# Kernel optimization log

Hardware: AMD Instinct MI355X
Metric: run time of the kernel (lower is better)

The kernel has to match this reference:

```python
import jax, jax.numpy as jnp
import numpy as np

ROPE_BASE = 10000.0

def _rope_cos_sin(T, d, dtype):
    inv_freq = 1.0 / (ROPE_BASE ** (jnp.arange(0, d, 2, dtype=jnp.float32) / d))
    t = jnp.arange(T, dtype=jnp.float32)
    freqs = t[:, None] * inv_freq[None, :]           # [T, d/2]
    emb = jnp.concatenate([freqs, freqs], axis=-1)   # [T, d]
    return jnp.cos(emb).astype(dtype), jnp.sin(emb).astype(dtype)

def _rotate_half(x):
    x1, x2 = jnp.split(x, 2, axis=-1)
    return jnp.concatenate([-x2, x1], axis=-1)

def setup_inputs() -> dict:
    key = jax.random.key(0)
    k1, k2, k3, k4 = jax.random.split(key, 4)
    B, T, C, H = 4, 4096, 1024, 64
    x = jax.random.normal(k1, (B, T, C), dtype=jnp.float32)
    s = 1.0 / np.sqrt(C)
    Wq = jax.random.normal(k2, (H, C), dtype=jnp.float32) * s
    Wk = jax.random.normal(k3, (H, C), dtype=jnp.float32) * s
    Wv = jax.random.normal(k4, (H, C), dtype=jnp.float32) * s
    return {"x": x, "Wq": Wq, "Wk": Wk, "Wv": Wv}

def reference(x, Wq, Wk, Wv):
    B, T, C = x.shape
    H = Wq.shape[0]
    q = jnp.einsum('btc,hc->bth', x, Wq)
    k = jnp.einsum('btc,hc->bth', x, Wk)
    v = jnp.einsum('btc,hc->bth', x, Wv)
    cos, sin = _rope_cos_sin(T, H, x.dtype)
    q = q * cos + _rotate_half(q) * sin
    k = k * cos + _rotate_half(k) * sin
    # NOTE: original scales by dim_model**-0.5 (C), not head_size
    wei = jnp.einsum('bth,bsh->bts', q, k) * (C ** -0.5)
    causal = jnp.tril(jnp.ones((T, T), dtype=bool))
    wei = jnp.where(causal, wei, -jnp.inf)
    wei = jax.nn.softmax(wei, axis=-1)
    # dropout p=0.0 (identity)
    out = jnp.einsum('bts,bsh->bth', wei, v)
    return out
```

## Files before the change

kernel.cpp:

```cpp
#include <hip/hip_runtime.h>
#include <hip/hip_bf16.h>
#include <math.h>

typedef __attribute__((ext_vector_type(8))) __bf16 bf16x8;
typedef __attribute__((ext_vector_type(4))) float f32x4;
typedef __attribute__((ext_vector_type(16))) float f32x16;
typedef __attribute__((ext_vector_type(4))) float float4_t;
typedef __attribute__((ext_vector_type(4))) unsigned int uint4_t;

#define NB 4
#define TSEQ 4096
#define CD 1024
#define HD 64
#define NCH 16
#define CHT 4
#define QBL 16

static __device__ __forceinline__ unsigned short f2bf(float f) {
    union { float f; unsigned u; } v; v.f = f;
    unsigned r = v.u + 0x7fffu + ((v.u >> 16) & 1u);
    return (unsigned short)(r >> 16);
}
static __device__ __forceinline__ float bf2f(unsigned short u) {
    union { unsigned int i; float f; } v; v.i = ((unsigned int)u) << 16;
    return v.f;
}
static __device__ __forceinline__ unsigned int pk2(float a, float b) {
    union { __bf16 h[2]; unsigned int u; } x;
    x.h[0] = (__bf16)a; x.h[1] = (__bf16)b;
    return x.u;
}

__global__ __launch_bounds__(256) void wcvt_kernel(const float* __restrict__ wq,
                                                   const float* __restrict__ wk,
                                                   const float* __restrict__ wv,
                                                   unsigned short* __restrict__ wb) {
    int i = blockIdx.x * 256 + threadIdx.x;
    int j = i >> 10;
    int col = i & 1023;
    int jb = j >> 4, off = j & 15;
    int sub = ((jb & 1) << 5) | ((jb & 2) << 3);
    int srcrow = (jb < 8) ? (sub + off) : ((jb - 8) * 16 + off);
    const float* src = (jb < 4) ? wq : ((jb < 8) ? wk : wv);
    wb[i] = f2bf(src[srcrow * 1024 + col]);
}

__global__ __launch_bounds__(256) void qkv_kernel(const float* __restrict__ x,
                                                  const unsigned short* __restrict__ wb,
                                                  unsigned short* __restrict__ qo,
                                                  unsigned short* __restrict__ ko,
                                                  unsigned short* __restrict__ vt) {
    __shared__ unsigned short xs[64][72];
    __shared__ unsigned short ws[64][72];
    const int tid = threadIdx.x;
    const int wave = tid >> 6, lane = tid & 63;
    const int lr = lane & 15;
    const int lk = (lane >> 4) << 3;
    const int rowg = (lane >> 4) << 2;
    const int row0 = blockIdx.x * 64;
    const int cbi = blockIdx.y;
    const int cb = cbi * 64;

    f32x4 acc[4];
#pragma unroll
    for (int i = 0; i < 4; ++i) acc[i] = (f32x4){0.f, 0.f, 0.f, 0.f};

    const int sr = tid >> 2;
    const int sc = (tid & 3) << 4;

    for (int k0 = 0; k0 < CD; k0 += 64) {
        __syncthreads();
        {
            const float4_t* s4 =
                reinterpret_cast<const float4_t*>(x + (size_t)(row0 + sr) * CD + k0 + sc);
            float4_t f0 = s4[0], f1 = s4[1], f2 = s4[2], f3 = s4[3];
            uint4_t w0, w1;
            w0[0] = pk2(f0[0], f0[1]); w0[1] = pk2(f0[2], f0[3]);
            w0[2] = pk2(f1[0], f1[1]); w0[3] = pk2(f1[2], f1[3]);
            w1[0] = pk2(f2[0], f2[1]); w1[1] = pk2(f2[2], f2[3]);
            w1[2] = pk2(f3[0], f3[1]); w1[3] = pk2(f3[2], f3[3]);
            *reinterpret_cast<uint4_t*>(&xs[sr][sc]) = w0;
            *reinterpret_cast<uint4_t*>(&xs[sr][sc + 8]) = w1;
        }
        {
            const uint4_t* wsrc =
                reinterpret_cast<const uint4_t*>(wb + (size_t)(cb + sr) * CD + k0 + sc);
            *reinterpret_cast<uint4_t*>(&ws[sr][sc]) = wsrc[0];
            *reinterpret_cast<uint4_t*>(&ws[sr][sc + 8]) = wsrc[1];
        }
        __syncthreads();
#pragma unroll
        for (int kk = 0; kk < 2; ++kk) {
            bf16x8 a = *reinterpret_cast<const bf16x8*>(&xs[wave * 16 + lr][kk * 32 + lk]);
#pragma unroll
            for (int c = 0; c < 4; ++c) {
                bf16x8 bfr = *reinterpret_cast<const bf16x8*>(&ws[c * 16 + lr][kk * 32 + lk]);
                acc[c] = __builtin_amdgcn_mfma_f32_16x16x32_bf16(a, bfr, acc[c], 0, 0, 0);
            }
        }
    }

    const int gr0 = row0 + wave * 16 + rowg;
    const int bidx = gr0 >> 12;
    const int tb = gr0 & (TSEQ - 1);
    if (cbi < 2) {
        unsigned short* o = (cbi == 0) ? qo : ko;
        const float sc2 = (cbi == 0) ? 0.045084218764560315f : 1.0f;
        const float l2b = 0.4152410118609215f;
        const float invf0 = exp2f(-(float)lr * l2b);
        const float invf1 = exp2f(-(float)(lr + 16) * l2b);
#pragma unroll
        for (int r = 0; r < 4; ++r) {
            float t = (float)(tb + r);
            float s0, c0, s1, c1;
            sincosf(t * invf0, &s0, &c0);
            sincosf(t * invf1, &s1, &c1);
            size_t ro = (size_t)(gr0 + r) * HD;
            float lo, hi;
            lo = acc[0][r]; hi = acc[1][r];
            o[ro + 0 + lr]  = f2bf((lo * c0 - hi * s0) * sc2);
            o[ro + 32 + lr] = f2bf((hi * c0 + lo * s0) * sc2);
            lo = acc[2][r]; hi = acc[3][r];
            o[ro + 16 + lr] = f2bf((lo * c1 - hi * s1) * sc2);
            o[ro + 48 + lr] = f2bf((hi * c1 + lo * s1) * sc2);
        }
    } else {
#pragma unroll
        for (int r = 0; r < 4; ++r) {
            size_t vbase = (size_t)bidx * HD * TSEQ + (size_t)(tb + r);
            vt[vbase + (size_t)(0 + lr) * TSEQ]  = f2bf(acc[0][r]);
            vt[vbase + (size_t)(16 + lr) * TSEQ] = f2bf(acc[1][r]);
            vt[vbase + (size_t)(32 + lr) * TSEQ] = f2bf(acc[2][r]);
            vt[vbase + (size_t)(48 + lr) * TSEQ] = f2bf(acc[3][r]);
        }
    }
}

__global__ __launch_bounds__(512, 4) void attn_partial(const unsigned short* __restrict__ q,
                                                       const unsigned short* __restrict__ k,
                                                       const unsigned short* __restrict__ vt,
                                                       unsigned short* __restrict__ po,
                                                       float* __restrict__ pm,
                                                       float* __restrict__ pl) {
    const int chunk = blockIdx.x, qb = blockIdx.y, b = blockIdx.z;
    const int ktend_blk = 4 * qb + 3;
    const int kt0 = chunk * CHT;
    if (kt0 > ktend_blk) return;
    const int ktend = min(ktend_blk, kt0 + CHT - 1);

    __shared__ unsigned short ks[64][72];
    __shared__ unsigned short vs[64][72];
    const int tid = threadIdx.x;
    const int wave = tid >> 6, lane = tid & 63;
    const int l31 = lane & 31;
    const int h = lane >> 5;
    const int h8 = h << 3;
    const int qrow0 = qb * 256 + wave * 32;
    const int qpos = qrow0 + l31;

    const unsigned short* qb_ = q + ((size_t)(b * TSEQ + qpos)) * HD + h8;
    bf16x8 qf[4];
#pragma unroll
    for (int s = 0; s < 4; ++s)
        qf[s] = *reinterpret_cast<const bf16x8*>(qb_ + 16 * s);

    f32x16 oacc[2];
#pragma unroll
    for (int dt = 0; dt < 2; ++dt)
#pragma unroll
        for (int r = 0; r < 16; ++r) oacc[dt][r] = 0.f;
    float mreg = -1.0e30f;
    float lsum = 0.f;

    const int srow = tid >> 3;
    const int scol = (tid & 7) << 3;
    const unsigned short* kbase = k + (size_t)b * TSEQ * HD;
    const unsigned short* vbase = vt + (size_t)b * HD * TSEQ;
    uint4_t kr, vr;

    auto loadtile = [&](int kt) {
        const int s0l = kt * 64;
        kr = *reinterpret_cast<const uint4_t*>(kbase + (size_t)(s0l + srow) * HD + scol);
        vr = *reinterpret_cast<const uint4_t*>(vbase + (size_t)srow * TSEQ + s0l + scol);
    };

    loadtile(kt0);

    for (int kt = kt0; kt <= ktend; ++kt) {
        const int s0 = kt * 64;
        __syncthreads();
        *reinterpret_cast<uint4_t*>(&ks[srow][scol]) = kr;
        *reinterpret_cast<uint4_t*>(&vs[srow][scol]) = vr;
        __syncthreads();
        if (kt < ktend) loadtile(kt + 1);

        if (s0 > qrow0 + 31) continue;

        f32x16 sacc[2];
#pragma unroll
        for (int blk = 0; blk < 2; ++blk)
#pragma unroll
            for (int r = 0; r < 16; ++r) sacc[blk][r] = 0.f;
        __builtin_amdgcn_s_setprio(1);
#pragma unroll
        for (int s = 0; s < 4; ++s) {
            bf16x8 ka = *reinterpret_cast<const bf16x8*>(&ks[l31][16 * s + h8]);
            bf16x8 kb2 = *reinterpret_cast<const bf16x8*>(&ks[32 + l31][16 * s + h8]);
            sacc[0] = __builtin_amdgcn_mfma_f32_32x32x16_bf16(ka, qf[s], sacc[0], 0, 0, 0);
            sacc[1] = __builtin_amdgcn_mfma_f32_32x32x16_bf16(kb2, qf[s], sacc[1], 0, 0, 0);
        }
        __builtin_amdgcn_s_setprio(0);

        if (s0 + 63 > qrow0) {
#pragma unroll
            for (int blk = 0; blk < 2; ++blk)
#pragma unroll
                for (int r = 0; r < 16; ++r) {
                    int kvpos = s0 + 32 * blk + (r & 3) + ((r >> 2) << 3) + (h << 2);
                    if (kvpos > qpos) sacc[blk][r] = -INFINITY;
                }
        }

        float tm[8];
#pragma unroll
        for (int r = 0; r < 8; ++r)
            tm[r] = fmaxf(fmaxf(sacc[0][r], sacc[0][r + 8]),
                          fmaxf(sacc[1][r], sacc[1][r + 8]));
#pragma unroll
        for (int r = 0; r < 4; ++r) tm[r] = fmaxf(tm[r], tm[r + 4]);
        float mx = fmaxf(fmaxf(tm[0], tm[1]), fmaxf(tm[2], tm[3]));
        mx = fmaxf(mx, __shfl_xor(mx, 32, 64));

        const bool newmax = !__all(mx <= mreg + 7.0f);
        if (newmax) {
            float mnew = fmaxf(mreg, mx);
            float corr = __builtin_amdgcn_exp2f(mreg - mnew);
            mreg = mnew;
            lsum *= corr;
#pragma unroll
            for (int dt = 0; dt < 2; ++dt)
#pragma unroll
                for (int r = 0; r < 16; ++r) oacc[dt][r] *= corr;
        }

        float pvv[2][16];
#pragma unroll
        for (int blk = 0; blk < 2; ++blk)
#pragma unroll
            for (int r = 0; r < 16; ++r)
                pvv[blk][r] = __builtin_amdgcn_exp2f(sacc[blk][r] - mreg);
        float ts[8];
#pragma unroll
        for (int r = 0; r < 8; ++r)
            ts[r] = (pvv[0][r] + pvv[0][r + 8]) + (pvv[1][r] + pvv[1][r + 8]);
#pragma unroll
        for (int r = 0; r < 4; ++r) ts[r] += ts[r + 4];
        float psum = (ts[0] + ts[1]) + (ts[2] + ts[3]);
        psum += __shfl_xor(psum, 32, 64);
        lsum += psum;

        unsigned int cw[2][4][2];
#pragma unroll
        for (int blk = 0; blk < 2; ++blk)
#pragma unroll
            for (int G = 0; G < 4; ++G) {
                cw[blk][G][0] = pk2(pvv[blk][4 * G], pvv[blk][4 * G + 1]);
                cw[blk][G][1] = pk2(pvv[blk][4 * G + 2], pvv[blk][4 * G + 3]);
            }

        const bool hif = (h == 1);
        __builtin_amdgcn_s_setprio(1);
#pragma unroll
        for (int s = 0; s < 4; ++s) {
            const int blk = s >> 1, base = (s & 1) << 1;
            unsigned int a0 = cw[blk][base][0],     a1 = cw[blk][base][1];
            unsigned int b0 = cw[blk][base + 1][0], b1 = cw[blk][base + 1][1];
            unsigned int s0w = hif ? a0 : b0;
            unsigned int s1w = hif ? a1 : b1;
            unsigned int r0 = __shfl_xor(s0w, 32, 64);
            unsigned int r1 = __shfl_xor(s1w, 32, 64);
            uint4_t pw;
            pw[0] = hif ? r0 : a0;
            pw[1] = hif ? r1 : a1;
            pw[2] = hif ? b0 : r0;
            pw[3] = hif ? b1 : r1;
            bf16x8 pfrag = *reinterpret_cast<const bf16x8*>(&pw);
            bf16x8 v0 = *reinterpret_cast<const bf16x8*>(&vs[l31][16 * s + h8]);
            bf16x8 v1 = *reinterpret_cast<const bf16x8*>(&vs[32 + l31][16 * s + h8]);
            oacc[0] = __builtin_amdgcn_mfma_f32_32x32x16_bf16(v0, pfrag, oacc[0], 0, 0, 0);
            oacc[1] = __builtin_amdgcn_mfma_f32_32x32x16_bf16(v1, pfrag, oacc[1], 0, 0, 0);
        }
        __builtin_amdgcn_s_setprio(0);
    }

    const int slot = (((b << 4) + qb) << 4) + chunk;
    unsigned short* pob = po + (size_t)slot * 16384;
#pragma unroll
    for (int dt = 0; dt < 2; ++dt)
#pragma unroll
        for (int r = 0; r < 16; ++r) {
            int d = 32 * dt + (r & 3) + ((r >> 2) << 3) + (h << 2);
            pob[d * 256 + wave * 32 + l31] = f2bf(oacc[dt][r]);
        }
    if (h == 0) {
        pm[slot * 256 + wave * 32 + l31] = mreg;
        pl[slot * 256 + wave * 32 + l31] = lsum;
    }
}

__global__ __launch_bounds__(256) void attn_combine(const unsigned short* __restrict__ po,
                                                    const float* __restrict__ pm,
                                                    const float* __restrict__ pl,
                                                    float* __restrict__ out) {
    __shared__ float sm[64][17];
    const int bq = blockIdx.x;
    const int dg = blockIdx.y;
    const int qt = bq & 63;
    const int b = bq >> 6;
    const int qb = qt >> 2, quarter = qt & 3;
    const int nch = qb + 1;
    const int qi = threadIdx.x & 63;
    const int jj = threadIdx.x >> 6;
    const int slotb = (((b << 4) + qb) << 4);
    const int qoff = quarter * 64 + qi;

    float pmv[NCH];
#pragma unroll
    for (int c = 0; c < NCH; ++c)
        pmv[c] = (c < nch) ? pm[(size_t)(slotb + c) * 256 + qoff] : -1.0e30f;
    float tmv[NCH];
#pragma unroll
    for (int c = 0; c < NCH; ++c) tmv[c] = pmv[c];
#pragma unroll
    for (int s = NCH / 2; s >= 1; s >>= 1)
#pragma unroll
        for (int c = 0; c < NCH / 2; ++c)
            if (c < s) tmv[c] = fmaxf(tmv[c], tmv[c + s]);
    const float M = tmv[0];

    float L = 0.f;
    float a0 = 0.f, a1 = 0.f, a2 = 0.f, a3 = 0.f;
    const int dbase = dg * 16 + jj * 4;
#pragma unroll 4
    for (int c = 0; c < nch; ++c) {
        float w = exp2f(pmv[c] - M);
        L += w * pl[(size_t)(slotb + c) * 256 + qoff];
        const unsigned short* p = po + (size_t)(slotb + c) * 16384 + dbase * 256 + qoff;
        a0 += w * bf2f(p[0]);
        a1 += w * bf2f(p[256]);
        a2 += w * bf2f(p[512]);
        a3 += w * bf2f(p[768]);
    }
    const float inv = 1.f / L;
    sm[qi][jj * 4 + 0] = a0 * inv;
    sm[qi][jj * 4 + 1] = a1 * inv;
    sm[qi][jj * 4 + 2] = a2 * inv;
    sm[qi][jj * 4 + 3] = a3 * inv;
    __syncthreads();
    const int row = threadIdx.x >> 2;
    const int c4 = (threadIdx.x & 3) << 2;
    float4_t f;
#pragma unroll
    for (int e = 0; e < 4; ++e) f[e] = sm[row][c4 + e];
    *reinterpret_cast<float4_t*>(out + (size_t)bq * 4096 + row * 64 + dg * 16 + c4) = f;
}

extern "C" void kernel_launch(void* const* d_in, const int* in_sizes, int n_in,
                              void* d_out, int out_size, void* d_ws, size_t ws_size,
                              hipStream_t stream) {
    const float* x = (const float*)d_in[0];
    const float* wq = (const float*)d_in[1];
    const float* wk = (const float*)d_in[2];
    const float* wv = (const float*)d_in[3];
    float* out = (float*)d_out;

    unsigned short* wb = (unsigned short*)d_ws;
    unsigned short* qb = wb + 3 * HD * CD;
    unsigned short* kb = qb + (size_t)NB * TSEQ * HD;
    unsigned short* vtb = kb + (size_t)NB * TSEQ * HD;
    unsigned short* pob = vtb + (size_t)NB * TSEQ * HD;
    float* pm = (float*)(pob + (size_t)1024 * 16384);
    float* pl = pm + (size_t)1024 * 256;

    wcvt_kernel<<<768, 256, 0, stream>>>(wq, wk, wv, wb);
    qkv_kernel<<<dim3(256, 3), 256, 0, stream>>>(x, wb, qb, kb, vtb);
    attn_partial<<<dim3(NCH, QBL, NB), 512, 0, stream>>>(qb, kb, vtb, pob, pm, pl);
    attn_combine<<<dim3(NB * 64, 4), 256, 0, stream>>>(pob, pm, pl, out);
}
```

Before: 63.25 us.

## Fuse weight conversion into QKV projection and split output into two 96-column phases

Removes the separate weight-conversion kernel. Weights are now read as fp32 and converted to bf16 inside the QKV projection. The projection grid shrinks from three 64-column blocks to two 96-column blocks, so x is re-read and re-converted twice instead of three times, and the RoPE outputs for Q/K are split across the two phases. In exchange, each block does more per-iteration weight loading and conversion from fp32, uses more accumulators, and launches fewer blocks.

After: 64.17 us. About the same (+1.5%).

```diff
diff --git a/kernel.cpp b/kernel.cpp
--- a/kernel.cpp
+++ b/kernel.cpp
@@ -31,42 +31,49 @@
     return x.u;
 }
 
-__global__ __launch_bounds__(256) void wcvt_kernel(const float* __restrict__ wq,
-                                                   const float* __restrict__ wk,
-                                                   const float* __restrict__ wv,
-                                                   unsigned short* __restrict__ wb) {
-    int i = blockIdx.x * 256 + threadIdx.x;
-    int j = i >> 10;
-    int col = i & 1023;
-    int jb = j >> 4, off = j & 15;
-    int sub = ((jb & 1) << 5) | ((jb & 2) << 3);
-    int srcrow = (jb < 8) ? (sub + off) : ((jb - 8) * 16 + off);
-    const float* src = (jb < 4) ? wq : ((jb < 8) ? wk : wv);
-    wb[i] = f2bf(src[srcrow * 1024 + col]);
-}
-
 __global__ __launch_bounds__(256) void qkv_kernel(const float* __restrict__ x,
-                                                  const unsigned short* __restrict__ wb,
+                                                  const float* __restrict__ wq,
+                                                  const float* __restrict__ wk,
+                                                  const float* __restrict__ wv,
                                                   unsigned short* __restrict__ qo,
                                                   unsigned short* __restrict__ ko,
                                                   unsigned short* __restrict__ vt) {
     __shared__ unsigned short xs[64][72];
-    __shared__ unsigned short ws[64][72];
+    __shared__ unsigned short ws[96][72];
     const int tid = threadIdx.x;
     const int wave = tid >> 6, lane = tid & 63;
     const int lr = lane & 15;
     const int lk = (lane >> 4) << 3;
     const int rowg = (lane >> 4) << 2;
     const int row0 = blockIdx.x * 64;
-    const int cbi = blockIdx.y;
-    const int cb = cbi * 64;
-
-    f32x4 acc[4];
-#pragma unroll
-    for (int i = 0; i < 4; ++i) acc[i] = (f32x4){0.f, 0.f, 0.f, 0.f};
+    const int phase = blockIdx.y;
+
+    f32x4 acc[6];
+#pragma unroll
+    for (int i = 0; i < 6; ++i) acc[i] = (f32x4){0.f, 0.f, 0.f, 0.f};
 
     const int sr = tid >> 2;
     const int sc = (tid & 3) << 4;
+
+    const float* wsrcp[3];
+    int wr_[3], wc_[3];
+#pragma unroll
+    for (int i = 0; i < 3; ++i) {
+        int u = tid + (i << 8);
+        int r = u >> 3, c = (u & 7) << 3;
+        wr_[i] = r; wc_[i] = c;
+        const float* srcp; int srcrow;
+        if (phase == 0) {
+            int jb = r >> 4, off = r & 15;
+            int sub = ((jb & 1) << 5) | ((jb & 2) << 3);
+            srcp = (jb < 4) ? wq : wk;
+            srcrow = sub + off;
+        } else {
+            if (r < 32) { srcp = wk; srcrow = 16 + ((r >> 4) << 5) + (r & 15); }
+            else        { srcp = wv; srcrow = r - 32; }
+        }
+        wsrcp[i] = srcp + (size_t)srcrow * CD + c;
+    }
 
     for (int k0 = 0; k0 < CD; k0 += 64) {
         __syncthreads();
@@ -82,18 +89,21 @@
             *reinterpret_cast<uint4_t*>(&xs[sr][sc]) = w0;
             *reinterpret_cast<uint4_t*>(&xs[sr][sc + 8]) = w1;
         }
-        {
-            const uint4_t* wsrc =
-                reinterpret_cast<const uint4_t*>(wb + (size_t)(cb + sr) * CD + k0 + sc);
-            *reinterpret_cast<uint4_t*>(&ws[sr][sc]) = wsrc[0];
-            *reinterpret_cast<uint4_t*>(&ws[sr][sc + 8]) = wsrc[1];
+#pragma unroll
+        for (int i = 0; i < 3; ++i) {
+            const float4_t* s4 = reinterpret_cast<const float4_t*>(wsrcp[i] + k0);
+            float4_t f0 = s4[0], f1 = s4[1];
+            uint4_t w;
+            w[0] = pk2(f0[0], f0[1]); w[1] = pk2(f0[2], f0[3]);
+            w[2] = pk2(f1[0], f1[1]); w[3] = pk2(f1[2], f1[3]);
+            *reinterpret_cast<uint4_t*>(&ws[wr_[i]][wc_[i]]) = w;
         }
         __syncthreads();
 #pragma unroll
         for (int kk = 0; kk < 2; ++kk) {
             bf16x8 a = *reinterpret_cast<const bf16x8*>(&xs[wave * 16 + lr][kk * 32 + lk]);
 #pragma unroll
-            for (int c = 0; c < 4; ++c) {
+            for (int c = 0; c < 6; ++c) {
                 bf16x8 bfr = *reinterpret_cast<const bf16x8*>(&ws[c * 16 + lr][kk * 32 + lk]);
                 acc[c] = __builtin_amdgcn_mfma_f32_16x16x32_bf16(a, bfr, acc[c], 0, 0, 0);
             }
@@ -103,35 +113,37 @@
     const int gr0 = row0 + wave * 16 + rowg;
     const int bidx = gr0 >> 12;
     const int tb = gr0 & (TSEQ - 1);
-    if (cbi < 2) {
-        unsigned short* o = (cbi == 0) ? qo : ko;
-        const float sc2 = (cbi == 0) ? 0.045084218764560315f : 1.0f;
-        const float l2b = 0.4152410118609215f;
-        const float invf0 = exp2f(-(float)lr * l2b);
-        const float invf1 = exp2f(-(float)(lr + 16) * l2b);
-#pragma unroll
-        for (int r = 0; r < 4; ++r) {
-            float t = (float)(tb + r);
-            float s0, c0, s1, c1;
-            sincosf(t * invf0, &s0, &c0);
-            sincosf(t * invf1, &s1, &c1);
-            size_t ro = (size_t)(gr0 + r) * HD;
+    const float sc2 = 0.045084218764560315f;
+    const float l2b = 0.4152410118609215f;
+    const float invf0 = exp2f(-(float)lr * l2b);
+    const float invf1 = exp2f(-(float)(lr + 16) * l2b);
+#pragma unroll
+    for (int r = 0; r < 4; ++r) {
+        float t = (float)(tb + r);
+        float s0, c0, s1, c1;
+        sincosf(t * invf0, &s0, &c0);
+        sincosf(t * invf1, &s1, &c1);
+        size_t ro = (size_t)(gr0 + r) * HD;
+        if (phase == 0) {
             float lo, hi;
             lo = acc[0][r]; hi = acc[1][r];
-            o[ro + 0 + lr]  = f2bf((lo * c0 - hi * s0) * sc2);
-            o[ro + 32 + lr] = f2bf((hi * c0 + lo * s0) * sc2);
+            qo[ro + 0 + lr]  = f2bf((lo * c0 - hi * s0) * sc2);
+            qo[ro + 32 + lr] = f2bf((hi * c0 + lo * s0) * sc2);
             lo = acc[2][r]; hi = acc[3][r];
-            o[ro + 16 + lr] = f2bf((lo * c1 - hi * s1) * sc2);
-            o[ro + 48 + lr] = f2bf((hi * c1 + lo * s1) * sc2);
-        }
-    } else {
-#pragma unroll
-        for (int r = 0; r < 4; ++r) {
+            qo[ro + 16 + lr] = f2bf((lo * c1 - hi * s1) * sc2);
+            qo[ro + 48 + lr] = f2bf((hi * c1 + lo * s1) * sc2);
+            lo = acc[4][r]; hi = acc[5][r];
+            ko[ro + 0 + lr]  = f2bf(lo * c0 - hi * s0);
+            ko[ro + 32 + lr] = f2bf(hi * c0 + lo * s0);
+        } else {
+            float lo = acc[0][r], hi = acc[1][r];
+            ko[ro + 16 + lr] = f2bf(lo * c1 - hi * s1);
+            ko[ro + 48 + lr] = f2bf(hi * c1 + lo * s1);
             size_t vbase = (size_t)bidx * HD * TSEQ + (size_t)(tb + r);
-            vt[vbase + (size_t)(0 + lr) * TSEQ]  = f2bf(acc[0][r]);
-            vt[vbase + (size_t)(16 + lr) * TSEQ] = f2bf(acc[1][r]);
-            vt[vbase + (size_t)(32 + lr) * TSEQ] = f2bf(acc[2][r]);
-            vt[vbase + (size_t)(48 + lr) * TSEQ] = f2bf(acc[3][r]);
+            vt[vbase + (size_t)(0 + lr) * TSEQ]  = f2bf(acc[2][r]);
+            vt[vbase + (size_t)(16 + lr) * TSEQ] = f2bf(acc[3][r]);
+            vt[vbase + (size_t)(32 + lr) * TSEQ] = f2bf(acc[4][r]);
+            vt[vbase + (size_t)(48 + lr) * TSEQ] = f2bf(acc[5][r]);
         }
     }
 }
@@ -374,16 +386,14 @@
     const float* wv = (const float*)d_in[3];
     float* out = (float*)d_out;
 
-    unsigned short* wb = (unsigned short*)d_ws;
-    unsigned short* qb = wb + 3 * HD * CD;
+    unsigned short* qb = (unsigned short*)d_ws;
     unsigned short* kb = qb + (size_t)NB * TSEQ * HD;
     unsigned short* vtb = kb + (size_t)NB * TSEQ * HD;
     unsigned short* pob = vtb + (size_t)NB * TSEQ * HD;
     float* pm = (float*)(pob + (size_t)1024 * 16384);
     float* pl = pm + (size_t)1024 * 256;
 
-    wcvt_kernel<<<768, 256, 0, stream>>>(wq, wk, wv, wb);
-    qkv_kernel<<<dim3(256, 3), 256, 0, stream>>>(x, wb, qb, kb, vtb);
+    qkv_kernel<<<dim3(256, 2), 256, 0, stream>>>(x, wq, wk, wv, qb, kb, vtb);
     attn_partial<<<dim3(NCH, QBL, NB), 512, 0, stream>>>(qb, kb, vtb, pob, pm, pl);
     attn_combine<<<dim3(NB * 64, 4), 256, 0, stream>>>(pob, pm, pl, out);
 }
```
